# Optimization experiments

Measured on AMD Instinct MI355X. Metric: run time of the kernel, lower is better.

The kernel has to match this reference:

```python
import jax, jax.numpy as jnp
import numpy as np

SIZE = 512          # framebuffer resolution (init kwarg `size`)
NUM_TRIS = 512      # number of triangles
EPS = 1e-9          # degenerate-triangle area threshold (matches `w < 1e-09`)


def setup_inputs() -> dict:
    key = jax.random.key(0)
    tris = jax.random.normal(key, (NUM_TRIS, 3, 3), dtype=jnp.float32)
    return {"tris": tris}


def _area2d(a, b, c):
    # signed parallelogram area: (b.x-a.x)*(c.y-a.y) - (b.y-a.y)*(c.x-a.x)
    return (b[..., 0] - a[..., 0]) * (c[..., 1] - a[..., 1]) - \
           (b[..., 1] - a[..., 1]) * (c[..., 0] - a[..., 0])


def reference(tris):
    size = SIZE
    dtype = tris.dtype
    half = jnp.asarray(size, dtype) * 0.5

    # lookup_table: pts[i, j] = (x_i, y_j), linspace(-1, 1), 'ij' indexing
    lin = jnp.linspace(-1.0, 1.0, size, dtype=dtype)
    xx, yy = jnp.meshgrid(lin, lin, indexing="ij")
    pts = jnp.stack([xx, yy], axis=-1)              # [S, S, 2]
    ii = jnp.arange(size)[:, None]                  # row index
    jj = jnp.arange(size)[None, :]                  # col index

    # zmin = min over all vertices of the z coordinate
    zmin = tris.reshape(-1, 3).min(axis=0)[2]
    zbuf0 = jnp.full((size, size), zmin, dtype=dtype)
    res0 = jnp.zeros((size, size, 4), dtype=dtype)

    def step(carry, tri):
        zbuf, res = carry
        t2 = tri[:, :2]                              # [3, 2] screen-space verts

        # AABB -> integer pixel box: clamp to [-1,1], map to [0,size], floor (long cast)
        aabb = jnp.concatenate([t2.min(axis=0), t2.max(axis=0)])  # xmin,ymin,xmax,ymax
        idx = jnp.floor((jnp.clip(aabb, -1.0, 1.0) + 1.0) * half).astype(jnp.int32)
        xmin, ymin, xmax, ymax = idx[0], idx[1], idx[2], idx[3]
        box = (ii >= xmin) & (ii < xmax) & (jj >= ymin) & (jj < ymax)

        w = _area2d(t2[0], t2[1], t2[2])
        valid = w >= EPS                              # original: skip if w < 1e-9
        ws = jnp.where(valid, w, jnp.asarray(1.0, dtype))

        # edge functions over the whole grid (the AABB slice only restricts pixels;
        # `box` reproduces that restriction exactly)
        pAB = _area2d(t2[1], pts, t2[0])
        pCB = _area2d(t2[2], pts, t2[1])
        pCA = _area2d(t2[0], pts, t2[2])
        inside = (jnp.maximum(pAB, 0.0) * jnp.maximum(pCB, 0.0) * jnp.maximum(pCA, 0.0)) > 0

        # barycentric interpolation of the 3d vertices
        w1 = pCB / ws
        w2 = pCA / ws
        w3 = 1.0 - w1 - w2
        p3 = w1[..., None] * tri[0] + w2[..., None] * tri[1] + w3[..., None] * tri[2]  # [S,S,3]

        zmsk = p3[..., 2] >= zbuf
        rmsk = inside & zmsk & box & valid

        zbuf = jnp.where(rmsk, p3[..., 2], zbuf)
        rgba = jnp.concatenate([p3, jnp.ones_like(p3[..., :1])], axis=-1)  # [S,S,4]
        res = jnp.where(rmsk[..., None], rgba, res)
        return (zbuf, res), None

    (zbuf, res), _ = jax.lax.scan(step, (zbuf0, res0), tris)
    return res
```

## Files before the change

### kernel.cpp

```cpp
#include <hip/hip_runtime.h>

#define TSIZE 512
#define NT 512
#define EPSV 1e-9f


__device__ __forceinline__ float rcp_fast(float x) {
  float r;
  asm("v_rcp_f32 %0, %1" : "=v"(r) : "v"(x));
  return r;
}

__global__ __launch_bounds__(512) void render_fused(const float* __restrict__ tris,
                                                    float4* __restrict__ out) {
  __shared__ float4 lrec[NT * 4];
  __shared__ unsigned lbY[NT];
  __shared__ float2 smrg[NT];
  __shared__ unsigned long long swords[32];
  __shared__ float sred[8];

  const int tid = threadIdx.x;
  const int bb = blockIdx.x;
  const int i = bb >> 1;
  const int jhalf = bb & 1;
  const unsigned jbase = (unsigned)(jhalf << 8);
  const float delta = 2.0f / 511.0f;

  {
    const float4* g4 = (const float4*)tris;
    float4* rw4 = lrec;
    rw4[tid] = g4[tid];
    rw4[tid + 512] = g4[tid + 512];
    if (tid < 128) rw4[tid + 1024] = g4[tid + 1024];
  }
  __syncthreads();

  const float* rawf = (const float*)lrec;
  const float* tp = rawf + tid * 9;
  float v0x = tp[0], v0y = tp[1], v0z = tp[2];
  float v1x = tp[3], v1y = tp[4], v1z = tp[5];
  float v2x = tp[6], v2y = tp[7], v2z = tp[8];
  __syncthreads();

  float w = __fsub_rn(__fmul_rn(__fsub_rn(v1x, v0x), __fsub_rn(v2y, v0y)),
                      __fmul_rn(__fsub_rn(v1y, v0y), __fsub_rn(v2x, v0x)));
  bool valid = (w >= EPSV);
  float ws = valid ? w : 1.0f;
  float r2  = __fsub_rn(v0y, v1y), r3  = __fsub_rn(v0x, v1x);
  float r6  = __fsub_rn(v1y, v2y), r7  = __fsub_rn(v1x, v2x);
  float r10 = __fsub_rn(v2y, v0y), r11 = __fsub_rn(v2x, v0x);

  int xmn = 0, xmx = 0, ymn = 0, ymx = 0;
  if (valid) {
    float bxn = fminf(v0x, fminf(v1x, v2x));
    float byn = fminf(v0y, fminf(v1y, v2y));
    float bxx = fmaxf(v0x, fmaxf(v1x, v2x));
    float byx = fmaxf(v0y, fmaxf(v1y, v2y));
    xmn = (int)floorf(__fmul_rn(__fadd_rn(fminf(fmaxf(bxn, -1.0f), 1.0f), 1.0f), 256.0f));
    ymn = (int)floorf(__fmul_rn(__fadd_rn(fminf(fmaxf(byn, -1.0f), 1.0f), 1.0f), 256.0f));
    xmx = (int)floorf(__fmul_rn(__fadd_rn(fminf(fmaxf(bxx, -1.0f), 1.0f), 1.0f), 256.0f));
    ymx = (int)floorf(__fmul_rn(__fadd_rn(fminf(fmaxf(byx, -1.0f), 1.0f), 1.0f), 256.0f));
  }

  const bool xpass = ((unsigned)i >= (unsigned)xmn) & ((unsigned)i < (unsigned)xmx);
  float ylo = -1e30f, yhi = 1e30f;
  if (xpass) {
    const float px_s = -1.0f + (float)i * delta;
    {
      float S = -r3, c = (v1y * r3 - v1x * r2) + r2 * px_s;
      if (S > 1e-20f)       { float cd = -c * rcp_fast(S); ylo = fmaxf(ylo, cd - (0.005f + 4e-6f * fabsf(cd))); }
      else if (S < -1e-20f) { float cd = -c * rcp_fast(S); yhi = fminf(yhi, cd + (0.005f + 4e-6f * fabsf(cd))); }
    }
    {
      float S = -r7, c = (v2y * r7 - v2x * r6) + r6 * px_s;
      if (S > 1e-20f)       { float cd = -c * rcp_fast(S); ylo = fmaxf(ylo, cd - (0.005f + 4e-6f * fabsf(cd))); }
      else if (S < -1e-20f) { float cd = -c * rcp_fast(S); yhi = fminf(yhi, cd + (0.005f + 4e-6f * fabsf(cd))); }
    }
    {
      float S = -r11, c = (v0y * r11 - v0x * r10) + r10 * px_s;
      if (S > 1e-20f)       { float cd = -c * rcp_fast(S); ylo = fmaxf(ylo, cd - (0.005f + 4e-6f * fabsf(cd))); }
      else if (S < -1e-20f) { float cd = -c * rcp_fast(S); yhi = fminf(yhi, cd + (0.005f + 4e-6f * fabsf(cd))); }
    }
  }

#pragma unroll
  for (int k = 0; k < 4; ++k) {
    const unsigned jw0 = jbase + ((unsigned)k << 6);
    const float pyL = -1.0f + (float)jw0 * delta;
    const float pyR = -1.0f + (float)(jw0 + 63u) * delta;
    bool pk = xpass & ((unsigned)ymn < jw0 + 64u) & ((unsigned)ymx > jw0) &
              (ylo <= pyR) & (yhi >= pyL);
    unsigned long long wd = __ballot(pk ? 1 : 0);
    if ((tid & 63) == 0) swords[k * 8 + (tid >> 6)] = wd;
  }

  lrec[tid * 4 + 0] = make_float4(v1x, v1y, r2, r3);
  lrec[tid * 4 + 1] = make_float4(v2x, v2y, r6, r7);
  lrec[tid * 4 + 2] = make_float4(v0x, v0y, r10, r11);
  lrec[tid * 4 + 3] = make_float4(__fdiv_rn(1.0f, ws), v2z,
                                  __fsub_rn(v0z, v2z), __fsub_rn(v1z, v2z));
  lbY[tid] = (unsigned)ymn | ((unsigned)ymx << 16);

  float zp = fminf(v0z, fminf(v1z, v2z));
  for (int off = 32; off > 0; off >>= 1) zp = fminf(zp, __shfl_down(zp, off, 64));
  if ((tid & 63) == 0) sred[tid >> 6] = zp;
  __syncthreads();
  float zm0 = sred[0];
#pragma unroll
  for (int kk = 1; kk < 8; ++kk) zm0 = fminf(zm0, sred[kk]);

  const int wv = tid >> 6;
  const int lane = tid & 63;
  const int k = wv >> 1;
  const int h = wv & 1;
  const unsigned ju = jbase + ((unsigned)k << 6) + (unsigned)lane;
  const float px = __fadd_rn(-1.0f, __fmul_rn((float)i, delta));
  const float py = __fadd_rn(-1.0f, __fmul_rn((float)ju, delta));

  float zb = zm0;
  int tw = -1;
#pragma unroll 1
  for (int q = 0; q < 4; ++q) {
    unsigned long long m = swords[k * 8 + h * 4 + q];
    const int tb = (h * 4 + q) << 6;
    while (m) {
      const int t = tb + __builtin_ctzll(m);
      m &= m - 1;
      float4 c0 = lrec[t * 4 + 0];
      float4 c1 = lrec[t * 4 + 1];
      float4 c2 = lrec[t * 4 + 2];
      float4 c3 = lrec[t * 4 + 3];
      unsigned yb = lbY[t];
      float pAB = __fsub_rn(__fmul_rn(__fsub_rn(px, c0.x), c0.z),
                            __fmul_rn(__fsub_rn(py, c0.y), c0.w));
      float pCB = __fsub_rn(__fmul_rn(__fsub_rn(px, c1.x), c1.z),
                            __fmul_rn(__fsub_rn(py, c1.y), c1.w));
      float pCA = __fsub_rn(__fmul_rn(__fsub_rn(px, c2.x), c2.z),
                            __fmul_rn(__fsub_rn(py, c2.y), c2.w));
      bool ins = (pAB > 0.0f) & (pCB > 0.0f) & (pCA > 0.0f) &
                 (ju >= (yb & 0xFFFFu)) & (ju < (yb >> 16));
      float w1 = __fmul_rn(pCB, c3.x);
      float w2 = __fmul_rn(pCA, c3.x);
      float pz = __fmaf_rn(w1, c3.z, __fmaf_rn(w2, c3.w, c3.y));
      bool mk = ins & (pz >= zb);
      zb = mk ? pz : zb;
      tw = mk ? t : tw;
    }
  }
  smrg[tid] = make_float2(zb, __int_as_float(tw));
  __syncthreads();

  if (tid < 256) {
    const int ks = tid >> 6, l = tid & 63;
    float2 a = smrg[ks * 128 + l];
    float2 b = smrg[ks * 128 + 64 + l];
    int t0 = __float_as_int(a.y), t1 = __float_as_int(b.y);
    bool win1 = (b.x > a.x) | ((b.x == a.x) & (t1 > t0));
    int twf = win1 ? t1 : t0;
    float zf = win1 ? b.x : a.x;

    const unsigned ju2 = jbase + (unsigned)tid;
    const float py2 = __fadd_rn(-1.0f, __fmul_rn((float)ju2, delta));

    float4 res = make_float4(0.0f, 0.0f, 0.0f, 0.0f);
    if (twf >= 0) {
      float4 f1 = lrec[twf * 4 + 1];
      float4 f2 = lrec[twf * 4 + 2];
      float4 f3 = lrec[twf * 4 + 3];
      float pCB = __fsub_rn(__fmul_rn(__fsub_rn(px, f1.x), f1.z),
                            __fmul_rn(__fsub_rn(py2, f1.y), f1.w));
      float pCA = __fsub_rn(__fmul_rn(__fsub_rn(px, f2.x), f2.z),
                            __fmul_rn(__fsub_rn(py2, f2.y), f2.w));
      float w1 = __fmul_rn(pCB, f3.x);
      float w2 = __fmul_rn(pCA, f3.x);
      float rx = __fmaf_rn(w1, -f2.w, __fmaf_rn(w2, f1.w, f1.x));
      float ry = __fmaf_rn(w1, -f2.z, __fmaf_rn(w2, f1.z, f1.y));
      res = make_float4(rx, ry, zf, 1.0f);
    }
    out[((unsigned)i << 9) | ju2] = res;
  }
}

extern "C" void kernel_launch(void* const* d_in, const int* in_sizes, int n_in,
                              void* d_out, int out_size, void* d_ws, size_t ws_size,
                              hipStream_t stream) {
  const float* tris = (const float*)d_in[0];
  float4* out = (float4*)d_out;
  hipLaunchKernelGGL(render_fused, dim3(1024), dim3(512), 0, stream, tris, out);
}
```

Baseline: 70.78 us.

## Process a full row per block with two pixels per thread

Each block now handles an entire 512-pixel row instead of half a row, and each thread evaluates two pixels 64 apart, reusing the x-dependent edge terms and the triangle loads from LDS across both. This halves the number of blocks, so the per-block setup (loading all triangles, binning, zmin reduction) runs half as often, and it amortizes the LDS reads per triangle. The trade-offs are coarser 128-pixel bins, so more triangles are tested per pixel, fewer blocks to fill the GPU, and a larger merge buffer.

```diff
diff --git a/kernel.cpp b/kernel.cpp
--- a/kernel.cpp
+++ b/kernel.cpp
@@ -15,15 +15,12 @@
                                                     float4* __restrict__ out) {
   __shared__ float4 lrec[NT * 4];
   __shared__ unsigned lbY[NT];
-  __shared__ float2 smrg[NT];
+  __shared__ float2 smrg[1024];
   __shared__ unsigned long long swords[32];
   __shared__ float sred[8];
 
   const int tid = threadIdx.x;
-  const int bb = blockIdx.x;
-  const int i = bb >> 1;
-  const int jhalf = bb & 1;
-  const unsigned jbase = (unsigned)(jhalf << 8);
+  const int i = blockIdx.x;
   const float delta = 2.0f / 511.0f;
 
   {
@@ -85,10 +82,10 @@
 
 #pragma unroll
   for (int k = 0; k < 4; ++k) {
-    const unsigned jw0 = jbase + ((unsigned)k << 6);
+    const unsigned jw0 = (unsigned)(k << 7);
     const float pyL = -1.0f + (float)jw0 * delta;
-    const float pyR = -1.0f + (float)(jw0 + 63u) * delta;
-    bool pk = xpass & ((unsigned)ymn < jw0 + 64u) & ((unsigned)ymx > jw0) &
+    const float pyR = -1.0f + (float)(jw0 + 127u) * delta;
+    bool pk = xpass & ((unsigned)ymn < jw0 + 128u) & ((unsigned)ymx > jw0) &
               (ylo <= pyR) & (yhi >= pyL);
     unsigned long long wd = __ballot(pk ? 1 : 0);
     if ((tid & 63) == 0) swords[k * 8 + (tid >> 6)] = wd;
@@ -113,12 +110,14 @@
   const int lane = tid & 63;
   const int k = wv >> 1;
   const int h = wv & 1;
-  const unsigned ju = jbase + ((unsigned)k << 6) + (unsigned)lane;
+  const unsigned ju0 = (unsigned)(k << 7) + (unsigned)lane;
+  const unsigned ju1 = ju0 + 64u;
   const float px = __fadd_rn(-1.0f, __fmul_rn((float)i, delta));
-  const float py = __fadd_rn(-1.0f, __fmul_rn((float)ju, delta));
-
-  float zb = zm0;
-  int tw = -1;
+  const float py0 = __fadd_rn(-1.0f, __fmul_rn((float)ju0, delta));
+  const float py1 = __fadd_rn(-1.0f, __fmul_rn((float)ju1, delta));
+
+  float zb0 = zm0, zb1 = zm0;
+  int tw0 = -1, tw1 = -1;
 #pragma unroll 1
   for (int q = 0; q < 4; ++q) {
     unsigned long long m = swords[k * 8 + h * 4 + q];
@@ -131,35 +130,52 @@
       float4 c2 = lrec[t * 4 + 2];
       float4 c3 = lrec[t * 4 + 3];
       unsigned yb = lbY[t];
-      float pAB = __fsub_rn(__fmul_rn(__fsub_rn(px, c0.x), c0.z),
-                            __fmul_rn(__fsub_rn(py, c0.y), c0.w));
-      float pCB = __fsub_rn(__fmul_rn(__fsub_rn(px, c1.x), c1.z),
-                            __fmul_rn(__fsub_rn(py, c1.y), c1.w));
-      float pCA = __fsub_rn(__fmul_rn(__fsub_rn(px, c2.x), c2.z),
-                            __fmul_rn(__fsub_rn(py, c2.y), c2.w));
-      bool ins = (pAB > 0.0f) & (pCB > 0.0f) & (pCA > 0.0f) &
-                 (ju >= (yb & 0xFFFFu)) & (ju < (yb >> 16));
-      float w1 = __fmul_rn(pCB, c3.x);
-      float w2 = __fmul_rn(pCA, c3.x);
-      float pz = __fmaf_rn(w1, c3.z, __fmaf_rn(w2, c3.w, c3.y));
-      bool mk = ins & (pz >= zb);
-      zb = mk ? pz : zb;
-      tw = mk ? t : tw;
-    }
-  }
-  smrg[tid] = make_float2(zb, __int_as_float(tw));
-  __syncthreads();
-
-  if (tid < 256) {
-    const int ks = tid >> 6, l = tid & 63;
-    float2 a = smrg[ks * 128 + l];
-    float2 b = smrg[ks * 128 + 64 + l];
+      const unsigned ym = yb & 0xFFFFu, yM = yb >> 16;
+      float eA = __fmul_rn(__fsub_rn(px, c0.x), c0.z);
+      float eB = __fmul_rn(__fsub_rn(px, c1.x), c1.z);
+      float eC = __fmul_rn(__fsub_rn(px, c2.x), c2.z);
+      {
+        float pAB = __fsub_rn(eA, __fmul_rn(__fsub_rn(py0, c0.y), c0.w));
+        float pCB = __fsub_rn(eB, __fmul_rn(__fsub_rn(py0, c1.y), c1.w));
+        float pCA = __fsub_rn(eC, __fmul_rn(__fsub_rn(py0, c2.y), c2.w));
+        bool ins = (pAB > 0.0f) & (pCB > 0.0f) & (pCA > 0.0f) &
+                   (ju0 >= ym) & (ju0 < yM);
+        float w1 = __fmul_rn(pCB, c3.x);
+        float w2 = __fmul_rn(pCA, c3.x);
+        float pz = __fmaf_rn(w1, c3.z, __fmaf_rn(w2, c3.w, c3.y));
+        bool mk = ins & (pz >= zb0);
+        zb0 = mk ? pz : zb0;
+        tw0 = mk ? t : tw0;
+      }
+      {
+        float pAB = __fsub_rn(eA, __fmul_rn(__fsub_rn(py1, c0.y), c0.w));
+        float pCB = __fsub_rn(eB, __fmul_rn(__fsub_rn(py1, c1.y), c1.w));
+        float pCA = __fsub_rn(eC, __fmul_rn(__fsub_rn(py1, c2.y), c2.w));
+        bool ins = (pAB > 0.0f) & (pCB > 0.0f) & (pCA > 0.0f) &
+                   (ju1 >= ym) & (ju1 < yM);
+        float w1 = __fmul_rn(pCB, c3.x);
+        float w2 = __fmul_rn(pCA, c3.x);
+        float pz = __fmaf_rn(w1, c3.z, __fmaf_rn(w2, c3.w, c3.y));
+        bool mk = ins & (pz >= zb1);
+        zb1 = mk ? pz : zb1;
+        tw1 = mk ? t : tw1;
+      }
+    }
+  }
+  smrg[k * 256 + h * 128 + lane] = make_float2(zb0, __int_as_float(tw0));
+  smrg[k * 256 + h * 128 + lane + 64] = make_float2(zb1, __int_as_float(tw1));
+  __syncthreads();
+
+  {
+    const int kp = tid >> 7, lp = tid & 127;
+    float2 a = smrg[kp * 256 + lp];
+    float2 b = smrg[kp * 256 + 128 + lp];
     int t0 = __float_as_int(a.y), t1 = __float_as_int(b.y);
     bool win1 = (b.x > a.x) | ((b.x == a.x) & (t1 > t0));
     int twf = win1 ? t1 : t0;
     float zf = win1 ? b.x : a.x;
 
-    const unsigned ju2 = jbase + (unsigned)tid;
+    const unsigned ju2 = (unsigned)tid;
     const float py2 = __fadd_rn(-1.0f, __fmul_rn((float)ju2, delta));
 
     float4 res = make_float4(0.0f, 0.0f, 0.0f, 0.0f);
@@ -186,5 +202,5 @@
                               hipStream_t stream) {
   const float* tris = (const float*)d_in[0];
   float4* out = (float4*)d_out;
-  hipLaunchKernelGGL(render_fused, dim3(1024), dim3(512), 0, stream, tris, out);
+  hipLaunchKernelGGL(render_fused, dim3(512), dim3(512), 0, stream, tris, out);
 }
```

Measured after the change: 72.33 us. +2.2%, slower.
